# Optimization experiments

Hardware: AMD Instinct MI355X
Metric: run time of the kernel (lower is better)

Reference implementation:

```python
import jax, jax.numpy as jnp
import numpy as np

N = 4096
IN_F = 512
OUT_F = 1024
HEADS = 8
HEAD_F = OUT_F // HEADS  # 128
NEG_SLOPE = 0.2


def setup_inputs() -> dict:
    key = jax.random.key(0)
    ks = jax.random.split(key, 7)
    x = jax.random.normal(ks[0], (N, IN_F), dtype=jnp.float32)
    graph = jax.random.randint(ks[1], (N, N), 0, 2, dtype=jnp.int32)
    # xavier-normal-ish init scales
    W = jax.random.normal(ks[2], (HEADS, IN_F, HEAD_F), dtype=jnp.float32) * (2.0 / (IN_F + HEAD_F)) ** 0.5
    w_i = jax.random.normal(ks[3], (HEADS, HEAD_F, 1), dtype=jnp.float32) * (2.0 / (HEAD_F + 1)) ** 0.5
    w_j = jax.random.normal(ks[4], (HEADS, HEAD_F, 1), dtype=jnp.float32) * (2.0 / (HEAD_F + 1)) ** 0.5
    W_r = jax.random.normal(ks[5], (IN_F, HEAD_F * HEADS), dtype=jnp.float32) * (2.0 / (IN_F + HEAD_F * HEADS)) ** 0.5
    bias = jnp.zeros((OUT_F,), dtype=jnp.float32)
    return {"x": x, "graph": graph, "W": W, "w_i": w_i, "w_j": w_j, "W_r": W_r, "bias": bias}


def reference(x, graph, W, w_i, w_j, W_r, bias):
    # h: [H, N, F] = x @ W per head
    h = jnp.einsum('nm,hmf->hnf', x, W)
    coe_i = jnp.einsum('hnf,hfo->hno', h, w_i)              # [H, N, 1]
    coe_j = jnp.einsum('hnf,hfo->hno', h, w_j).transpose(0, 2, 1)  # [H, 1, N]
    coe = jax.nn.leaky_relu(coe_i + coe_j, negative_slope=NEG_SLOPE)  # [H, N, N]
    # adjacency mask: note the transpose as in the original (graph.t())
    mask = jnp.where(graph.T > 0, 0.0, -jnp.inf).astype(h.dtype)  # [N, N]
    att = jax.nn.softmax(coe + mask[None], axis=-1)          # [H, N, N]
    y = jnp.einsum('hnm,hmf->nhf', att, h)                   # [N, H, F]
    # mapped residual (in_features != head_features)
    y = y + (x @ W_r).reshape(-1, HEADS, HEAD_F)
    # concat heads
    y = y.reshape(-1, OUT_F)
    return y + bias
```

## Files before the change

### kernel.cpp

```cpp
#include <hip/hip_runtime.h>
#include <hip/hip_fp16.h>

typedef _Float16 f16;
typedef _Float16 f16x8 __attribute__((ext_vector_type(8)));
typedef _Float16 f16x2v __attribute__((ext_vector_type(2)));
typedef __fp16 h16x2 __attribute__((ext_vector_type(2)));
typedef float f32x4 __attribute__((ext_vector_type(4)));
typedef float f32x16 __attribute__((ext_vector_type(16)));

#define LOG2E 1.4426950408889634f
#define NSL 0.2f

__global__ __launch_bounds__(256) void k_a(const float* __restrict__ x,
                                           f16* __restrict__ xh2,
                                           const float* __restrict__ W,
                                           f16* __restrict__ Wht2,
                                           const float* __restrict__ Wr,
                                           f16* __restrict__ Wrt2,
                                           unsigned int* __restrict__ M2e) {
    __shared__ float tile[32][33];
    int bx = blockIdx.x;
    int tid = threadIdx.x;
    if (bx == 0 && tid < 8) M2e[tid] = 0x007FFFFFu;
    if (bx < 512) {
        int id = bx * 256 + tid;
        int row = id & 4095, kt = id >> 12;
        const float4* xs = (const float4*)(x + (size_t)row * 512 + kt * 16);
        float4 u0 = xs[0], u1 = xs[1], u2 = xs[2], u3 = xs[3];
        union { int4 a[2]; h16x2 p[8]; } px;
        px.p[0] = __builtin_amdgcn_cvt_pkrtz(u0.x, u0.y);
        px.p[1] = __builtin_amdgcn_cvt_pkrtz(u0.z, u0.w);
        px.p[2] = __builtin_amdgcn_cvt_pkrtz(u1.x, u1.y);
        px.p[3] = __builtin_amdgcn_cvt_pkrtz(u1.z, u1.w);
        px.p[4] = __builtin_amdgcn_cvt_pkrtz(u2.x, u2.y);
        px.p[5] = __builtin_amdgcn_cvt_pkrtz(u2.z, u2.w);
        px.p[6] = __builtin_amdgcn_cvt_pkrtz(u3.x, u3.y);
        px.p[7] = __builtin_amdgcn_cvt_pkrtz(u3.z, u3.w);
        int4* d = (int4*)(xh2 + ((size_t)kt * 4096 + row) * 16);
        d[0] = px.a[0]; d[1] = px.a[1];
    } else {
        const float* in; f16* out; int C, S, bxx, byy;
        if (bx < 1024) { int id = bx - 512;  in = W;  out = Wht2; C = 128;  S = 128;  bxx = id & 3;  byy = id >> 2; }
        else           { int id = bx - 1024; in = Wr; out = Wrt2; C = 1024; S = 1024; bxx = id & 31; byy = id >> 5; }
        int tx = tid & 31, ty = tid >> 5;
        int c0 = bxx * 32, r0 = byy * 32;
        for (int rr = ty; rr < 32; rr += 8)
            tile[rr][tx] = in[(r0 + rr) * C + c0 + tx];
        __syncthreads();
        for (int rr = ty; rr < 32; rr += 8) {
            int m = r0 + tx, f = c0 + rr;
            out[(size_t)((m >> 4) * S + f) * 16 + (m & 15)] = (f16)tile[tx][rr];
        }
    }
}

__global__ __launch_bounds__(256, 4) void k_b(const f16* __restrict__ xh2,
                                              const f16* __restrict__ Wht2,
                                              f16* __restrict__ hbT2,
                                              const float* __restrict__ wi,
                                              const float* __restrict__ wj,
                                              float* __restrict__ a2,
                                              float* __restrict__ b2,
                                              unsigned int* __restrict__ M2e,
                                              const int* __restrict__ graph,
                                              unsigned int* __restrict__ maskJ) {
    __shared__ float swi[128], swj[128];
    __shared__ float pwa[4][32], pwb[4][32];
    __shared__ unsigned long long bal[4][64];
    int bx = blockIdx.x;
    int tid = threadIdx.x;
    int w = tid >> 6, lane = tid & 63;

    if (bx >= 1024) {
        int gw = (bx - 1024) * 4 + w;
        int ti = gw & 63, tj = gw >> 6;
        int i0 = ti * 64, j0 = tj * 64;
        #pragma unroll 8
        for (int k = 0; k < 64; k++) {
            int g = graph[(j0 + k) * 4096 + i0 + lane];
            unsigned long long b = __ballot(g > 0);
            if (lane == 0) bal[w][k] = b;
        }
        __syncthreads();
        unsigned long long word = 0;
        #pragma unroll 8
        for (int k = 0; k < 64; k++) {
            word |= ((bal[w][k] >> lane) & 1ull) << k;
        }
        int jw = j0 >> 5;
        maskJ[(size_t)jw * 4096 + i0 + lane]       = (unsigned int)word;
        maskJ[(size_t)(jw + 1) * 4096 + i0 + lane] = (unsigned int)(word >> 32);
        return;
    }

    int h = bx & 7, jb = bx >> 3;
    int j0 = jb * 32;
    int ln = lane & 15, q = lane >> 4;
    if (tid < 128) { swi[tid] = wi[h * 128 + tid]; swj[tid] = wj[h * 128 + tid]; }
    __syncthreads();

    int ko = (q & 1) * 8;
    const f16* pa = Wht2 + ((size_t)(h * 512) * 8 + (size_t)(q >> 1) * 128 + w * 32 + ln) * 16 + ko;
    const f16* pb = xh2 + ((size_t)(q >> 1) * 4096 + j0 + ln) * 16 + ko;

    f32x4 acc00 = {}, acc01 = {}, acc10 = {}, acc11 = {};

    f16x8 ra0 = *(const f16x8*)(pa);
    f16x8 ra1 = *(const f16x8*)(pa + 256);
    f16x8 rb0 = *(const f16x8*)(pb);
    f16x8 rb1 = *(const f16x8*)(pb + 256);

    for (int kk = 0; kk < 8; kk++) {
        f16x8 sa0 = *(const f16x8*)(pa + 4096);
        f16x8 sa1 = *(const f16x8*)(pa + 4096 + 256);
        f16x8 sb0 = *(const f16x8*)(pb + 131072);
        f16x8 sb1 = *(const f16x8*)(pb + 131072 + 256);
        acc00 = __builtin_amdgcn_mfma_f32_16x16x32_f16(ra0, rb0, acc00, 0, 0, 0);
        acc01 = __builtin_amdgcn_mfma_f32_16x16x32_f16(ra0, rb1, acc01, 0, 0, 0);
        acc10 = __builtin_amdgcn_mfma_f32_16x16x32_f16(ra1, rb0, acc10, 0, 0, 0);
        acc11 = __builtin_amdgcn_mfma_f32_16x16x32_f16(ra1, rb1, acc11, 0, 0, 0);
        pa += 8192; pb += 262144;
        ra0 = *(const f16x8*)(pa);
        ra1 = *(const f16x8*)(pa + 256);
        rb0 = *(const f16x8*)(pb);
        rb1 = *(const f16x8*)(pb + 256);
        acc00 = __builtin_amdgcn_mfma_f32_16x16x32_f16(sa0, sb0, acc00, 0, 0, 0);
        acc01 = __builtin_amdgcn_mfma_f32_16x16x32_f16(sa0, sb1, acc01, 0, 0, 0);
        acc10 = __builtin_amdgcn_mfma_f32_16x16x32_f16(sa1, sb0, acc10, 0, 0, 0);
        acc11 = __builtin_amdgcn_mfma_f32_16x16x32_f16(sa1, sb1, acc11, 0, 0, 0);
    }

    size_t hb = (size_t)h * 524288 + (size_t)(j0 >> 4) * 2048;
    #pragma unroll
    for (int r = 0; r < 4; r++) {
        int f0 = w * 32 + q * 4 + r;
        hbT2[hb + f0 * 16 + ln]                 = (f16)acc00[r];
        hbT2[hb + 2048 + f0 * 16 + ln]          = (f16)acc01[r];
        hbT2[hb + (f0 + 16) * 16 + ln]          = (f16)acc10[r];
        hbT2[hb + 2048 + (f0 + 16) * 16 + ln]   = (f16)acc11[r];
    }

    float pa0 = 0.f, pb0 = 0.f, pa1 = 0.f, pb1 = 0.f;
    #pragma unroll
    for (int r = 0; r < 4; r++) {
        int f0 = w * 32 + q * 4 + r;
        float w0 = swi[f0], jv0 = swj[f0];
        float w1 = swi[f0 + 16], jv1 = swj[f0 + 16];
        pa0 += acc00[r] * w0 + acc10[r] * w1;
        pb0 += acc00[r] * jv0 + acc10[r] * jv1;
        pa1 += acc01[r] * w0 + acc11[r] * w1;
        pb1 += acc01[r] * jv0 + acc11[r] * jv1;
    }
    pa0 += __shfl_xor(pa0, 16); pa0 += __shfl_xor(pa0, 32);
    pb0 += __shfl_xor(pb0, 16); pb0 += __shfl_xor(pb0, 32);
    pa1 += __shfl_xor(pa1, 16); pa1 += __shfl_xor(pa1, 32);
    pb1 += __shfl_xor(pb1, 16); pb1 += __shfl_xor(pb1, 32);
    if (lane < 16) {
        pwa[w][ln] = pa0;      pwb[w][ln] = pb0;
        pwa[w][16 + ln] = pa1; pwb[w][16 + ln] = pb1;
    }
    __syncthreads();
    if (tid < 32) {
        int jj = tid;
        float pav = (pwa[0][jj] + pwa[1][jj]) + (pwa[2][jj] + pwa[3][jj]);
        float pbv = (pwb[0][jj] + pwb[1][jj]) + (pwb[2][jj] + pwb[3][jj]);
        a2[h * 4096 + j0 + jj] = pav * LOG2E;
        float bb = pbv * LOG2E;
        b2[h * 4096 + j0 + jj] = bb;
        float m = bb;
        m = fmaxf(m, __shfl_xor(m, 1, 32));
        m = fmaxf(m, __shfl_xor(m, 2, 32));
        m = fmaxf(m, __shfl_xor(m, 4, 32));
        m = fmaxf(m, __shfl_xor(m, 8, 32));
        m = fmaxf(m, __shfl_xor(m, 16, 32));
        if (jj == 0) {
            unsigned u = __float_as_uint(m);
            unsigned enc = (u & 0x80000000u) ? ~u : (u | 0x80000000u);
            atomicMax(&M2e[h], enc);
        }
    }
}

#define PGEN2(af, m8, qv, qw)                                                        \
    {                                                                                \
        union { int4 i4; unsigned u[4]; } uv, uw;                                    \
        uv.i4 = (qv); uw.i4 = (qw);                                                  \
        f16x2v dl = {(_Float16)0, (_Float16)0};                                      \
        _Pragma("unroll")                                                            \
        for (int p = 0; p < 4; p++) {                                                \
            union { unsigned u; f16x2v v; } b1, b2x, mm;                             \
            b1.u = uv.u[p]; b2x.u = uw.u[p];                                         \
            f16x2v pr1 = Ap1 * b1.v;                                                 \
            f16x2v pr2 = Ap2 * b2x.v;                                                \
            mm.v = __builtin_elementwise_max(pr1, pr2);                              \
            int mlo = -(int)(((m8) >> (2 * p)) & 1u);                                \
            int mhi = -(int)(((m8) >> (2 * p + 1)) & 1u);                            \
            unsigned comb = ((unsigned)mlo & 0xFFFFu) | ((unsigned)mhi & 0xFFFF0000u);\
            mm.u &= comb;                                                            \
            af.u[p] = mm.u;                                                          \
            dl += mm.v;                                                              \
        }                                                                            \
        dsum += (float)dl.x + (float)dl.y;                                           \
    }

#define PUTACC(dp, off, accv)                                                    \
    {                                                                            \
        union { f32x16 v; f32x4 q[4]; } t; t.v = (accv);                         \
        *(f32x4*)((dp) + (off))      = t.q[0];                                   \
        *(f32x4*)((dp) + (off) + 4)  = t.q[1];                                   \
        *(f32x4*)((dp) + (off) + 8)  = t.q[2];                                   \
        *(f32x4*)((dp) + (off) + 12) = t.q[3];                                   \
    }

#define ADDACC(dp, off, accv)                                                    \
    {                                                                            \
        union { f32x16 v; f32x4 q[4]; } t; t.v = (accv);                         \
        t.q[0] += *(const f32x4*)((dp) + (off));                                 \
        t.q[1] += *(const f32x4*)((dp) + (off) + 4);                             \
        t.q[2] += *(const f32x4*)((dp) + (off) + 8);                             \
        t.q[3] += *(const f32x4*)((dp) + (off) + 12);                            \
        (accv) = t.v;                                                            \
    }

__global__ __launch_bounds__(256, 4) void k_main(const f16* __restrict__ xh2,
                                                 const f16* __restrict__ hbT2,
                                                 const f16* __restrict__ Wrt2,
                                                 const unsigned int* __restrict__ maskJ,
                                                 const float* __restrict__ a2,
                                                 const float* __restrict__ b2,
                                                 const unsigned int* __restrict__ M2e,
                                                 const float* __restrict__ bias,
                                                 float* __restrict__ out) {
    __shared__ char smem[35328];
    __shared__ float dred[128];

    unsigned int* mlds = (unsigned int*)smem;
    unsigned int* bvlds = (unsigned int*)(smem + 16512);
    unsigned int* bwlds = (unsigned int*)(smem + 24704);

    int bx = blockIdx.x;
    int h = bx & 7, it = bx >> 3;
    int i0 = it * 32;
    int tid = threadIdx.x;
    int w = tid >> 6, lane = tid & 63;
    int l31 = lane & 31, half = lane >> 5;
    int i = i0 + l31;

    unsigned enc = M2e[h];
    unsigned um = (enc & 0x80000000u) ? (enc & 0x7FFFFFFFu) : ~enc;
    float M2 = __uint_as_float(um);

    {
        const float2* bsrc = (const float2*)(b2 + h * 4096);
        #pragma unroll
        for (int c = 0; c < 8; c++) {
            int p = tid + c * 256;
            float2 tb = bsrc[p];
            float t0 = tb.x - M2, t1 = tb.y - M2;
            union { h16x2 pp; unsigned ii; } k1, k2;
            k1.pp = __builtin_amdgcn_cvt_pkrtz(exp2f(t0), exp2f(t1));
            k2.pp = __builtin_amdgcn_cvt_pkrtz(exp2f(NSL * t0), exp2f(NSL * t1));
            bvlds[p] = k1.ii;
            bwlds[p] = k2.ii;
        }
        #pragma unroll
        for (int c = 0; c < 16; c++) {
            int e = tid + c * 256;
            int jw = e >> 5, ii = e & 31;
            mlds[ii * 129 + jw] = maskJ[(size_t)jw * 4096 + i0 + ii];
        }
    }

    float av = a2[h * 4096 + i];
    float uu = av + M2;
    float m2v = fmaxf(uu, NSL * uu);
    union { h16x2 pp; f16x2v v; } apk;
    apk.pp = __builtin_amdgcn_cvt_pkrtz(exp2f(uu - m2v), exp2f(NSL * uu - m2v));
    f16x2v Ap1 = {apk.v.x, apk.v.x};
    f16x2v Ap2 = {apk.v.y, apk.v.y};

    f32x16 acc0 = {}, acc1 = {}, acc2 = {}, acc3 = {};
    float dsum = 0.f;

    int J0 = w * 1024;
    const f16* bb = hbT2 + (size_t)h * 524288 + ((size_t)(J0 >> 4) * 128 + l31) * 16 + half * 8;
    const unsigned int* bpv = bvlds + (J0 >> 1) + half * 4;
    const unsigned int* bpw = bwlds + (J0 >> 1) + half * 4;
    const unsigned int* mrow = mlds + l31 * 129 + (J0 >> 5);

    int sh0 = half << 3;
    int sh1 = 16 + (half << 3);

    __syncthreads();

    f16x8 fa0 = *(const f16x8*)(bb);
    f16x8 fa1 = *(const f16x8*)(bb + 512);
    f16x8 fa2 = *(const f16x8*)(bb + 1024);
    f16x8 fa3 = *(const f16x8*)(bb + 1536);
    int4 qv0 = ((const int4*)(bpv))[0];
    int4 qw0 = ((const int4*)(bpw))[0];
    unsigned mwc = mrow[0];

    for (int tp = 0; tp < 32; tp++) {
        int t0 = tp * 2;
        const f16* s1 = bb + (size_t)(t0 + 1) * 2048;
        f16x8 fb0 = *(const f16x8*)(s1);
        f16x8 fb1 = *(const f16x8*)(s1 + 512);
        f16x8 fb2 = *(const f16x8*)(s1 + 1024);
        f16x8 fb3 = *(const f16x8*)(s1 + 1536);
        int4 qv1 = *(const int4*)(bpv + (t0 + 1) * 8);
        int4 qw1 = *(const int4*)(bpw + (t0 + 1) * 8);
        unsigned mwn = mrow[tp + 1];

        {
            union { f16x8 v; unsigned u[4]; } af;
            PGEN2(af, mwc >> sh0, qv0, qw0);
            acc0 = __builtin_amdgcn_mfma_f32_32x32x16_f16(af.v, fa0, acc0, 0, 0, 0);
            acc1 = __builtin_amdgcn_mfma_f32_32x32x16_f16(af.v, fa1, acc1, 0, 0, 0);
            acc2 = __builtin_amdgcn_mfma_f32_32x32x16_f16(af.v, fa2, acc2, 0, 0, 0);
            acc3 = __builtin_amdgcn_mfma_f32_32x32x16_f16(af.v, fa3, acc3, 0, 0, 0);
        }

        const f16* s2 = bb + (size_t)(t0 + 2) * 2048;
        fa0 = *(const f16x8*)(s2);
        fa1 = *(const f16x8*)(s2 + 512);
        fa2 = *(const f16x8*)(s2 + 1024);
        fa3 = *(const f16x8*)(s2 + 1536);
        qv0 = *(const int4*)(bpv + (t0 + 2) * 8);
        qw0 = *(const int4*)(bpw + (t0 + 2) * 8);

        {
            union { f16x8 v; unsigned u[4]; } af;
            PGEN2(af, mwc >> sh1, qv1, qw1);
            acc0 = __builtin_amdgcn_mfma_f32_32x32x16_f16(af.v, fb0, acc0, 0, 0, 0);
            acc1 = __builtin_amdgcn_mfma_f32_32x32x16_f16(af.v, fb1, acc1, 0, 0, 0);
            acc2 = __builtin_amdgcn_mfma_f32_32x32x16_f16(af.v, fb2, acc2, 0, 0, 0);
            acc3 = __builtin_amdgcn_mfma_f32_32x32x16_f16(af.v, fb3, acc3, 0, 0, 0);
        }
        mwc = mwn;
    }

    dsum += __shfl(dsum, lane ^ 32);
    if (lane < 32) dred[w * 32 + l31] = dsum;
    __syncthreads();
    {
        #pragma unroll
        for (int r = 0; r < 16; r++) {
            int row = (r & 3) + 8 * (r >> 2) + 4 * half;
            float s = dred[row] + dred[32 + row] + dred[64 + row] + dred[96 + row];
            float inv = 1.0f / s;
            acc0[r] *= inv; acc1[r] *= inv; acc2[r] *= inv; acc3[r] *= inv;
        }
    }

    {
        #pragma unroll
        for (int kt = 0; kt < 8; kt++) {
            int ktt = w * 8 + kt;
            f16x8 ax = *(const f16x8*)(xh2 + ((size_t)ktt * 4096 + i) * 16 + half * 8);
            const f16* wb = Wrt2 + ((size_t)ktt * 1024 + h * 128 + l31) * 16 + half * 8;
            acc0 = __builtin_amdgcn_mfma_f32_32x32x16_f16(ax, *(const f16x8*)(wb), acc0, 0, 0, 0);
            acc1 = __builtin_amdgcn_mfma_f32_32x32x16_f16(ax, *(const f16x8*)(wb + 512), acc1, 0, 0, 0);
            acc2 = __builtin_amdgcn_mfma_f32_32x32x16_f16(ax, *(const f16x8*)(wb + 1024), acc2, 0, 0, 0);
            acc3 = __builtin_amdgcn_mfma_f32_32x32x16_f16(ax, *(const f16x8*)(wb + 1536), acc3, 0, 0, 0);
        }
    }

    float* xredb = (float*)smem;
    __syncthreads();
    if (w >= 2) {
        float* dp = xredb + (w - 2) * 4352 + lane * 68;
        PUTACC(dp, 0, acc0); PUTACC(dp, 16, acc1); PUTACC(dp, 32, acc2); PUTACC(dp, 48, acc3);
    }
    __syncthreads();
    if (w < 2) {
        const float* dp = xredb + w * 4352 + lane * 68;
        ADDACC(dp, 0, acc0); ADDACC(dp, 16, acc1); ADDACC(dp, 32, acc2); ADDACC(dp, 48, acc3);
    }
    __syncthreads();
    if (w == 1) {
        float* dp = xredb + lane * 68;
        PUTACC(dp, 0, acc0); PUTACC(dp, 16, acc1); PUTACC(dp, 32, acc2); PUTACC(dp, 48, acc3);
    }
    __syncthreads();
    if (w == 0) {
        const float* dp = xredb + lane * 68;
        ADDACC(dp, 0, acc0); ADDACC(dp, 16, acc1); ADDACC(dp, 32, acc2); ADDACC(dp, 48, acc3);
        #pragma unroll
        for (int n = 0; n < 4; n++) {
            union { f32x16 v; f32x4 q[4]; } t;
            t.v = (n == 0) ? acc0 : (n == 1) ? acc1 : (n == 2) ? acc2 : acc3;
            int col = h * 128 + n * 32 + l31;
            float bv = bias[col];
            #pragma unroll
            for (int r = 0; r < 16; r++) {
                int row = i0 + (r & 3) + 8 * (r >> 2) + 4 * half;
                out[(size_t)row * 1024 + col] = t.v[r] + bv;
            }
        }
    }
}

extern "C" void kernel_launch(void* const* d_in, const int* in_sizes, int n_in,
                              void* d_out, int out_size, void* d_ws, size_t ws_size,
                              hipStream_t stream) {
    (void)in_sizes; (void)n_in; (void)out_size; (void)ws_size;
    const float* x     = (const float*)d_in[0];
    const int*   graph = (const int*)d_in[1];
    const float* W     = (const float*)d_in[2];
    const float* wi    = (const float*)d_in[3];
    const float* wj    = (const float*)d_in[4];
    const float* Wr    = (const float*)d_in[5];
    const float* bias  = (const float*)d_in[6];
    float* out = (float*)d_out;

    char* ws = (char*)d_ws;
    unsigned int* maskJ = (unsigned int*)ws;
    f16* hbT2  = (f16*)(ws + (2u << 20));
    f16* Wht2  = (f16*)(ws + (10u << 20));
    f16* Wrt2  = (f16*)(ws + (11u << 20));
    f16* xh2   = (f16*)(ws + (12u << 20));
    float* a2    = (float*)(ws + (16u << 20));
    float* b2    = a2 + 8 * 4096;
    unsigned int* M2e = (unsigned int*)(b2 + 8 * 4096);

    hipLaunchKernelGGL(k_a, dim3(1536), dim3(256), 0, stream, x, xh2, W, Wht2, Wr, Wrt2, M2e);
    hipLaunchKernelGGL(k_b, dim3(2048), dim3(256), 0, stream, xh2, Wht2, hbT2,
                       wi, wj, a2, b2, M2e, graph, maskJ);
    hipLaunchKernelGGL(k_main, dim3(1024), dim3(256), 0, stream, xh2, hbT2, Wrt2, maskJ,
                       a2, b2, M2e, bias, out);
}
```

Baseline: 222.6 us.

## Process 64 query rows per block to reuse loaded h tiles twice

Each k_main block now handles 64 rows instead of 32, with two sets of MFMA accumulators (low and high halves) sharing the same B fragments of hbT2 and the same exp tables held in LDS. This halves the global traffic for the value matrix and the per-block exp-table setup, and halves the grid to 512 blocks. In exchange, register pressure doubles, which forces launch bounds down to 2 blocks per SM. LDS use also grows, and with fewer blocks on a 256-CU part occupancy and load balance may suffer.

```diff
diff --git a/kernel.cpp b/kernel.cpp
--- a/kernel.cpp
+++ b/kernel.cpp
@@ -181,7 +181,7 @@
     }
 }
 
-#define PGEN2(af, m8, qv, qw)                                                        \
+#define PGEN2(af, m8, qv, qw, A1, A2, DS)                                            \
     {                                                                                \
         union { int4 i4; unsigned u[4]; } uv, uw;                                    \
         uv.i4 = (qv); uw.i4 = (qw);                                                  \
@@ -190,8 +190,8 @@
         for (int p = 0; p < 4; p++) {                                                \
             union { unsigned u; f16x2v v; } b1, b2x, mm;                             \
             b1.u = uv.u[p]; b2x.u = uw.u[p];                                         \
-            f16x2v pr1 = Ap1 * b1.v;                                                 \
-            f16x2v pr2 = Ap2 * b2x.v;                                                \
+            f16x2v pr1 = (A1) * b1.v;                                                \
+            f16x2v pr2 = (A2) * b2x.v;                                               \
             mm.v = __builtin_elementwise_max(pr1, pr2);                              \
             int mlo = -(int)(((m8) >> (2 * p)) & 1u);                                \
             int mhi = -(int)(((m8) >> (2 * p + 1)) & 1u);                            \
@@ -200,7 +200,7 @@
             af.u[p] = mm.u;                                                          \
             dl += mm.v;                                                              \
         }                                                                            \
-        dsum += (float)dl.x + (float)dl.y;                                           \
+        DS += (float)dl.x + (float)dl.y;                                             \
     }
 
 #define PUTACC(dp, off, accv)                                                    \
@@ -222,7 +222,7 @@
         (accv) = t.v;                                                            \
     }
 
-__global__ __launch_bounds__(256, 4) void k_main(const f16* __restrict__ xh2,
+__global__ __launch_bounds__(256, 2) void k_main(const f16* __restrict__ xh2,
                                                  const f16* __restrict__ hbT2,
                                                  const f16* __restrict__ Wrt2,
                                                  const unsigned int* __restrict__ maskJ,
@@ -231,16 +231,16 @@
                                                  const unsigned int* __restrict__ M2e,
                                                  const float* __restrict__ bias,
                                                  float* __restrict__ out) {
-    __shared__ char smem[35328];
-    __shared__ float dred[128];
+    __shared__ char smem[49664];
+    __shared__ float dred[256];
 
     unsigned int* mlds = (unsigned int*)smem;
-    unsigned int* bvlds = (unsigned int*)(smem + 16512);
-    unsigned int* bwlds = (unsigned int*)(smem + 24704);
+    unsigned int* bvlds = (unsigned int*)(smem + 33024);
+    unsigned int* bwlds = (unsigned int*)(smem + 41216);
 
     int bx = blockIdx.x;
     int h = bx & 7, it = bx >> 3;
-    int i0 = it * 32;
+    int i0 = it * 64;
     int tid = threadIdx.x;
     int w = tid >> 6, lane = tid & 63;
     int l31 = lane & 31, half = lane >> 5;
@@ -264,29 +264,36 @@
             bwlds[p] = k2.ii;
         }
         #pragma unroll
-        for (int c = 0; c < 16; c++) {
+        for (int c = 0; c < 32; c++) {
             int e = tid + c * 256;
-            int jw = e >> 5, ii = e & 31;
+            int jw = e >> 6, ii = e & 63;
             mlds[ii * 129 + jw] = maskJ[(size_t)jw * 4096 + i0 + ii];
         }
     }
 
-    float av = a2[h * 4096 + i];
-    float uu = av + M2;
-    float m2v = fmaxf(uu, NSL * uu);
-    union { h16x2 pp; f16x2v v; } apk;
-    apk.pp = __builtin_amdgcn_cvt_pkrtz(exp2f(uu - m2v), exp2f(NSL * uu - m2v));
-    f16x2v Ap1 = {apk.v.x, apk.v.x};
-    f16x2v Ap2 = {apk.v.y, apk.v.y};
-
-    f32x16 acc0 = {}, acc1 = {}, acc2 = {}, acc3 = {};
-    float dsum = 0.f;
+    float avL = a2[h * 4096 + i];
+    float avH = a2[h * 4096 + i + 32];
+    float uuL = avL + M2, uuH = avH + M2;
+    float mvL = fmaxf(uuL, NSL * uuL);
+    float mvH = fmaxf(uuH, NSL * uuH);
+    union { h16x2 pp; f16x2v v; } apL, apH;
+    apL.pp = __builtin_amdgcn_cvt_pkrtz(exp2f(uuL - mvL), exp2f(NSL * uuL - mvL));
+    apH.pp = __builtin_amdgcn_cvt_pkrtz(exp2f(uuH - mvH), exp2f(NSL * uuH - mvH));
+    f16x2v ApL1 = {apL.v.x, apL.v.x};
+    f16x2v ApL2 = {apL.v.y, apL.v.y};
+    f16x2v ApH1 = {apH.v.x, apH.v.x};
+    f16x2v ApH2 = {apH.v.y, apH.v.y};
+
+    f32x16 accL0 = {}, accL1 = {}, accL2 = {}, accL3 = {};
+    f32x16 accH0 = {}, accH1 = {}, accH2 = {}, accH3 = {};
+    float dsumL = 0.f, dsumH = 0.f;
 
     int J0 = w * 1024;
     const f16* bb = hbT2 + (size_t)h * 524288 + ((size_t)(J0 >> 4) * 128 + l31) * 16 + half * 8;
     const unsigned int* bpv = bvlds + (J0 >> 1) + half * 4;
     const unsigned int* bpw = bwlds + (J0 >> 1) + half * 4;
-    const unsigned int* mrow = mlds + l31 * 129 + (J0 >> 5);
+    const unsigned int* mrowL = mlds + l31 * 129 + (J0 >> 5);
+    const unsigned int* mrowH = mlds + (l31 + 32) * 129 + (J0 >> 5);
 
     int sh0 = half << 3;
     int sh1 = 16 + (half << 3);
@@ -299,7 +306,8 @@
     f16x8 fa3 = *(const f16x8*)(bb + 1536);
     int4 qv0 = ((const int4*)(bpv))[0];
     int4 qw0 = ((const int4*)(bpw))[0];
-    unsigned mwc = mrow[0];
+    unsigned mwcL = mrowL[0];
+    unsigned mwcH = mrowH[0];
 
     for (int tp = 0; tp < 32; tp++) {
         int t0 = tp * 2;
@@ -310,15 +318,24 @@
         f16x8 fb3 = *(const f16x8*)(s1 + 1536);
         int4 qv1 = *(const int4*)(bpv + (t0 + 1) * 8);
         int4 qw1 = *(const int4*)(bpw + (t0 + 1) * 8);
-        unsigned mwn = mrow[tp + 1];
+        unsigned mwnL = mrowL[tp + 1];
+        unsigned mwnH = mrowH[tp + 1];
 
         {
             union { f16x8 v; unsigned u[4]; } af;
-            PGEN2(af, mwc >> sh0, qv0, qw0);
-            acc0 = __builtin_amdgcn_mfma_f32_32x32x16_f16(af.v, fa0, acc0, 0, 0, 0);
-            acc1 = __builtin_amdgcn_mfma_f32_32x32x16_f16(af.v, fa1, acc1, 0, 0, 0);
-            acc2 = __builtin_amdgcn_mfma_f32_32x32x16_f16(af.v, fa2, acc2, 0, 0, 0);
-            acc3 = __builtin_amdgcn_mfma_f32_32x32x16_f16(af.v, fa3, acc3, 0, 0, 0);
+            PGEN2(af, mwcL >> sh0, qv0, qw0, ApL1, ApL2, dsumL);
+            accL0 = __builtin_amdgcn_mfma_f32_32x32x16_f16(af.v, fa0, accL0, 0, 0, 0);
+            accL1 = __builtin_amdgcn_mfma_f32_32x32x16_f16(af.v, fa1, accL1, 0, 0, 0);
+            accL2 = __builtin_amdgcn_mfma_f32_32x32x16_f16(af.v, fa2, accL2, 0, 0, 0);
+            accL3 = __builtin_amdgcn_mfma_f32_32x32x16_f16(af.v, fa3, accL3, 0, 0, 0);
+        }
+        {
+            union { f16x8 v; unsigned u[4]; } af;
+            PGEN2(af, mwcH >> sh0, qv0, qw0, ApH1, ApH2, dsumH);
+            accH0 = __builtin_amdgcn_mfma_f32_32x32x16_f16(af.v, fa0, accH0, 0, 0, 0);
+            accH1 = __builtin_amdgcn_mfma_f32_32x32x16_f16(af.v, fa1, accH1, 0, 0, 0);
+            accH2 = __builtin_amdgcn_mfma_f32_32x32x16_f16(af.v, fa2, accH2, 0, 0, 0);
+            accH3 = __builtin_amdgcn_mfma_f32_32x32x16_f16(af.v, fa3, accH3, 0, 0, 0);
         }
 
         const f16* s2 = bb + (size_t)(t0 + 2) * 2048;
@@ -331,25 +348,41 @@
 
         {
             union { f16x8 v; unsigned u[4]; } af;
-            PGEN2(af, mwc >> sh1, qv1, qw1);
-            acc0 = __builtin_amdgcn_mfma_f32_32x32x16_f16(af.v, fb0, acc0, 0, 0, 0);
-            acc1 = __builtin_amdgcn_mfma_f32_32x32x16_f16(af.v, fb1, acc1, 0, 0, 0);
-            acc2 = __builtin_amdgcn_mfma_f32_32x32x16_f16(af.v, fb2, acc2, 0, 0, 0);
-            acc3 = __builtin_amdgcn_mfma_f32_32x32x16_f16(af.v, fb3, acc3, 0, 0, 0);
-        }
-        mwc = mwn;
-    }
-
-    dsum += __shfl(dsum, lane ^ 32);
-    if (lane < 32) dred[w * 32 + l31] = dsum;
+            PGEN2(af, mwcL >> sh1, qv1, qw1, ApL1, ApL2, dsumL);
+            accL0 = __builtin_amdgcn_mfma_f32_32x32x16_f16(af.v, fb0, accL0, 0, 0, 0);
+            accL1 = __builtin_amdgcn_mfma_f32_32x32x16_f16(af.v, fb1, accL1, 0, 0, 0);
+            accL2 = __builtin_amdgcn_mfma_f32_32x32x16_f16(af.v, fb2, accL2, 0, 0, 0);
+            accL3 = __builtin_amdgcn_mfma_f32_32x32x16_f16(af.v, fb3, accL3, 0, 0, 0);
+        }
+        {
+            union { f16x8 v; unsigned u[4]; } af;
+            PGEN2(af, mwcH >> sh1, qv1, qw1, ApH1, ApH2, dsumH);
+            accH0 = __builtin_amdgcn_mfma_f32_32x32x16_f16(af.v, fb0, accH0, 0, 0, 0);
+            accH1 = __builtin_amdgcn_mfma_f32_32x32x16_f16(af.v, fb1, accH1, 0, 0, 0);
+            accH2 = __builtin_amdgcn_mfma_f32_32x32x16_f16(af.v, fb2, accH2, 0, 0, 0);
+            accH3 = __builtin_amdgcn_mfma_f32_32x32x16_f16(af.v, fb3, accH3, 0, 0, 0);
+        }
+        mwcL = mwnL;
+        mwcH = mwnH;
+    }
+
+    dsumL += __shfl(dsumL, lane ^ 32);
+    dsumH += __shfl(dsumH, lane ^ 32);
+    if (lane < 32) {
+        dred[w * 64 + l31] = dsumL;
+        dred[w * 64 + 32 + l31] = dsumH;
+    }
     __syncthreads();
     {
         #pragma unroll
         for (int r = 0; r < 16; r++) {
             int row = (r & 3) + 8 * (r >> 2) + 4 * half;
-            float s = dred[row] + dred[32 + row] + dred[64 + row] + dred[96 + row];
-            float inv = 1.0f / s;
-            acc0[r] *= inv; acc1[r] *= inv; acc2[r] *= inv; acc3[r] *= inv;
+            float sL = dred[row] + dred[64 + row] + dred[128 + row] + dred[192 + row];
+            float sH = dred[32 + row] + dred[96 + row] + dred[160 + row] + dred[224 + row];
+            float invL = 1.0f / sL;
+            float invH = 1.0f / sH;
+            accL0[r] *= invL; accL1[r] *= invL; accL2[r] *= invL; accL3[r] *= invL;
+            accH0[r] *= invH; accH1[r] *= invH; accH2[r] *= invH; accH3[r] *= invH;
         }
     }
 
@@ -357,44 +390,87 @@
         #pragma unroll
         for (int kt = 0; kt < 8; kt++) {
             int ktt = w * 8 + kt;
-            f16x8 ax = *(const f16x8*)(xh2 + ((size_t)ktt * 4096 + i) * 16 + half * 8);
+            f16x8 axL = *(const f16x8*)(xh2 + ((size_t)ktt * 4096 + i) * 16 + half * 8);
+            f16x8 axH = *(const f16x8*)(xh2 + ((size_t)ktt * 4096 + i + 32) * 16 + half * 8);
             const f16* wb = Wrt2 + ((size_t)ktt * 1024 + h * 128 + l31) * 16 + half * 8;
-            acc0 = __builtin_amdgcn_mfma_f32_32x32x16_f16(ax, *(const f16x8*)(wb), acc0, 0, 0, 0);
-            acc1 = __builtin_amdgcn_mfma_f32_32x32x16_f16(ax, *(const f16x8*)(wb + 512), acc1, 0, 0, 0);
-            acc2 = __builtin_amdgcn_mfma_f32_32x32x16_f16(ax, *(const f16x8*)(wb + 1024), acc2, 0, 0, 0);
-            acc3 = __builtin_amdgcn_mfma_f32_32x32x16_f16(ax, *(const f16x8*)(wb + 1536), acc3, 0, 0, 0);
+            f16x8 wb0 = *(const f16x8*)(wb);
+            f16x8 wb1 = *(const f16x8*)(wb + 512);
+            f16x8 wb2 = *(const f16x8*)(wb + 1024);
+            f16x8 wb3 = *(const f16x8*)(wb + 1536);
+            accL0 = __builtin_amdgcn_mfma_f32_32x32x16_f16(axL, wb0, accL0, 0, 0, 0);
+            accL1 = __builtin_amdgcn_mfma_f32_32x32x16_f16(axL, wb1, accL1, 0, 0, 0);
+            accL2 = __builtin_amdgcn_mfma_f32_32x32x16_f16(axL, wb2, accL2, 0, 0, 0);
+            accL3 = __builtin_amdgcn_mfma_f32_32x32x16_f16(axL, wb3, accL3, 0, 0, 0);
+            accH0 = __builtin_amdgcn_mfma_f32_32x32x16_f16(axH, wb0, accH0, 0, 0, 0);
+            accH1 = __builtin_amdgcn_mfma_f32_32x32x16_f16(axH, wb1, accH1, 0, 0, 0);
+            accH2 = __builtin_amdgcn_mfma_f32_32x32x16_f16(axH, wb2, accH2, 0, 0, 0);
+            accH3 = __builtin_amdgcn_mfma_f32_32x32x16_f16(axH, wb3, accH3, 0, 0, 0);
         }
     }
 
     float* xredb = (float*)smem;
+
     __syncthreads();
     if (w >= 2) {
         float* dp = xredb + (w - 2) * 4352 + lane * 68;
-        PUTACC(dp, 0, acc0); PUTACC(dp, 16, acc1); PUTACC(dp, 32, acc2); PUTACC(dp, 48, acc3);
+        PUTACC(dp, 0, accL0); PUTACC(dp, 16, accL1); PUTACC(dp, 32, accL2); PUTACC(dp, 48, accL3);
     }
     __syncthreads();
     if (w < 2) {
         const float* dp = xredb + w * 4352 + lane * 68;
-        ADDACC(dp, 0, acc0); ADDACC(dp, 16, acc1); ADDACC(dp, 32, acc2); ADDACC(dp, 48, acc3);
+        ADDACC(dp, 0, accL0); ADDACC(dp, 16, accL1); ADDACC(dp, 32, accL2); ADDACC(dp, 48, accL3);
     }
     __syncthreads();
     if (w == 1) {
         float* dp = xredb + lane * 68;
-        PUTACC(dp, 0, acc0); PUTACC(dp, 16, acc1); PUTACC(dp, 32, acc2); PUTACC(dp, 48, acc3);
+        PUTACC(dp, 0, accL0); PUTACC(dp, 16, accL1); PUTACC(dp, 32, accL2); PUTACC(dp, 48, accL3);
     }
     __syncthreads();
     if (w == 0) {
         const float* dp = xredb + lane * 68;
-        ADDACC(dp, 0, acc0); ADDACC(dp, 16, acc1); ADDACC(dp, 32, acc2); ADDACC(dp, 48, acc3);
+        ADDACC(dp, 0, accL0); ADDACC(dp, 16, accL1); ADDACC(dp, 32, accL2); ADDACC(dp, 48, accL3);
         #pragma unroll
         for (int n = 0; n < 4; n++) {
             union { f32x16 v; f32x4 q[4]; } t;
-            t.v = (n == 0) ? acc0 : (n == 1) ? acc1 : (n == 2) ? acc2 : acc3;
+            t.v = (n == 0) ? accL0 : (n == 1) ? accL1 : (n == 2) ? accL2 : accL3;
             int col = h * 128 + n * 32 + l31;
             float bv = bias[col];
             #pragma unroll
             for (int r = 0; r < 16; r++) {
                 int row = i0 + (r & 3) + 8 * (r >> 2) + 4 * half;
+                out[(size_t)row * 1024 + col] = t.v[r] + bv;
+            }
+        }
+    }
+
+    __syncthreads();
+    if (w >= 2) {
+        float* dp = xredb + (w - 2) * 4352 + lane * 68;
+        PUTACC(dp, 0, accH0); PUTACC(dp, 16, accH1); PUTACC(dp, 32, accH2); PUTACC(dp, 48, accH3);
+    }
+    __syncthreads();
+    if (w < 2) {
+        const float* dp = xredb + w * 4352 + lane * 68;
+        ADDACC(dp, 0, accH0); ADDACC(dp, 16, accH1); ADDACC(dp, 32, accH2); ADDACC(dp, 48, accH3);
+    }
+    __syncthreads();
+    if (w == 1) {
+        float* dp = xredb + lane * 68;
+        PUTACC(dp, 0, accH0); PUTACC(dp, 16, accH1); PUTACC(dp, 32, accH2); PUTACC(dp, 48, accH3);
+    }
+    __syncthreads();
+    if (w == 0) {
+        const float* dp = xredb + lane * 68;
+        ADDACC(dp, 0, accH0); ADDACC(dp, 16, accH1); ADDACC(dp, 32, accH2); ADDACC(dp, 48, accH3);
+        #pragma unroll
+        for (int n = 0; n < 4; n++) {
+            union { f32x16 v; f32x4 q[4]; } t;
+            t.v = (n == 0) ? accH0 : (n == 1) ? accH1 : (n == 2) ? accH2 : accH3;
+            int col = h * 128 + n * 32 + l31;
+            float bv = bias[col];
+            #pragma unroll
+            for (int r = 0; r < 16; r++) {
+                int row = i0 + 32 + (r & 3) + 8 * (r >> 2) + 4 * half;
                 out[(size_t)row * 1024 + col] = t.v[r] + bv;
             }
         }
@@ -427,6 +503,6 @@
     hipLaunchKernelGGL(k_a, dim3(1536), dim3(256), 0, stream, x, xh2, W, Wht2, Wr, Wrt2, M2e);
     hipLaunchKernelGGL(k_b, dim3(2048), dim3(256), 0, stream, xh2, Wht2, hbT2,
                        wi, wj, a2, b2, M2e, graph, maskJ);
-    hipLaunchKernelGGL(k_main, dim3(1024), dim3(256), 0, stream, xh2, hbT2, Wrt2, maskJ,
+    hipLaunchKernelGGL(k_main, dim3(512), dim3(256), 0, stream, xh2, hbT2, Wrt2, maskJ,
                        a2, b2, M2e, bias, out);
 }
```

Result: faster. 210.7 us (-5.4%).

## Restructure attention kernel to share probability tiles via LDS across 8 waves

Applied to the files above, without the earlier changes.

The main attention kernel now uses 512-thread blocks covering 64 rows. Each wave generates a slice of the masked softmax probabilities into double-buffered LDS, and all waves then run MFMAs on a 32-row by 32-feature output tile. The old per-wave split over the key dimension is gone, and with it the cross-wave accumulator reduction through LDS. The mask-packing path in k_b now does a per-thread strided gather instead of a ballot-and-transpose, with more blocks launched. This trades fewer redundant probability computations and smaller reductions for a barrier on every chunk and more LDS traffic.

```diff
diff --git a/kernel.cpp b/kernel.cpp
--- a/kernel.cpp
+++ b/kernel.cpp
@@ -66,30 +66,21 @@
                                               unsigned int* __restrict__ maskJ) {
     __shared__ float swi[128], swj[128];
     __shared__ float pwa[4][32], pwb[4][32];
-    __shared__ unsigned long long bal[4][64];
     int bx = blockIdx.x;
     int tid = threadIdx.x;
     int w = tid >> 6, lane = tid & 63;
 
     if (bx >= 1024) {
-        int gw = (bx - 1024) * 4 + w;
-        int ti = gw & 63, tj = gw >> 6;
-        int i0 = ti * 64, j0 = tj * 64;
-        #pragma unroll 8
-        for (int k = 0; k < 64; k++) {
-            int g = graph[(j0 + k) * 4096 + i0 + lane];
-            unsigned long long b = __ballot(g > 0);
-            if (lane == 0) bal[w][k] = b;
-        }
-        __syncthreads();
-        unsigned long long word = 0;
-        #pragma unroll 8
-        for (int k = 0; k < 64; k++) {
-            word |= ((bal[w][k] >> lane) & 1ull) << k;
-        }
-        int jw = j0 >> 5;
-        maskJ[(size_t)jw * 4096 + i0 + lane]       = (unsigned int)word;
-        maskJ[(size_t)(jw + 1) * 4096 + i0 + lane] = (unsigned int)(word >> 32);
+        int e = (bx - 1024) * 256 + tid;
+        int jw = e >> 12, ii = e & 4095;
+        const int* gp = graph + (size_t)(jw << 5) * 4096 + ii;
+        int gv[32];
+        #pragma unroll
+        for (int k = 0; k < 32; k++) gv[k] = gp[(size_t)k * 4096];
+        unsigned word = 0;
+        #pragma unroll
+        for (int k = 0; k < 32; k++) word |= (gv[k] > 0) ? (1u << k) : 0u;
+        maskJ[e] = word;
         return;
     }
 
@@ -181,7 +172,7 @@
     }
 }
 
-#define PGEN2(af, m8, qv, qw)                                                        \
+#define PGEN2(af, m8, qv, qw, A1, A2, DS)                                            \
     {                                                                                \
         union { int4 i4; unsigned u[4]; } uv, uw;                                    \
         uv.i4 = (qv); uw.i4 = (qw);                                                  \
@@ -190,8 +181,8 @@
         for (int p = 0; p < 4; p++) {                                                \
             union { unsigned u; f16x2v v; } b1, b2x, mm;                             \
             b1.u = uv.u[p]; b2x.u = uw.u[p];                                         \
-            f16x2v pr1 = Ap1 * b1.v;                                                 \
-            f16x2v pr2 = Ap2 * b2x.v;                                                \
+            f16x2v pr1 = (A1) * b1.v;                                                \
+            f16x2v pr2 = (A2) * b2x.v;                                               \
             mm.v = __builtin_elementwise_max(pr1, pr2);                              \
             int mlo = -(int)(((m8) >> (2 * p)) & 1u);                                \
             int mhi = -(int)(((m8) >> (2 * p + 1)) & 1u);                            \
@@ -200,29 +191,10 @@
             af.u[p] = mm.u;                                                          \
             dl += mm.v;                                                              \
         }                                                                            \
-        dsum += (float)dl.x + (float)dl.y;                                           \
-    }
-
-#define PUTACC(dp, off, accv)                                                    \
-    {                                                                            \
-        union { f32x16 v; f32x4 q[4]; } t; t.v = (accv);                         \
-        *(f32x4*)((dp) + (off))      = t.q[0];                                   \
-        *(f32x4*)((dp) + (off) + 4)  = t.q[1];                                   \
-        *(f32x4*)((dp) + (off) + 8)  = t.q[2];                                   \
-        *(f32x4*)((dp) + (off) + 12) = t.q[3];                                   \
-    }
-
-#define ADDACC(dp, off, accv)                                                    \
-    {                                                                            \
-        union { f32x16 v; f32x4 q[4]; } t; t.v = (accv);                         \
-        t.q[0] += *(const f32x4*)((dp) + (off));                                 \
-        t.q[1] += *(const f32x4*)((dp) + (off) + 4);                             \
-        t.q[2] += *(const f32x4*)((dp) + (off) + 8);                             \
-        t.q[3] += *(const f32x4*)((dp) + (off) + 12);                            \
-        (accv) = t.v;                                                            \
-    }
-
-__global__ __launch_bounds__(256, 4) void k_main(const f16* __restrict__ xh2,
+        DS += (float)dl.x + (float)dl.y;                                             \
+    }
+
+__global__ __launch_bounds__(512, 4) void k_main(const f16* __restrict__ xh2,
                                                  const f16* __restrict__ hbT2,
                                                  const f16* __restrict__ Wrt2,
                                                  const unsigned int* __restrict__ maskJ,
@@ -232,19 +204,25 @@
                                                  const float* __restrict__ bias,
                                                  float* __restrict__ out) {
     __shared__ char smem[35328];
-    __shared__ float dred[128];
-
-    unsigned int* mlds = (unsigned int*)smem;
-    unsigned int* bvlds = (unsigned int*)(smem + 16512);
-    unsigned int* bwlds = (unsigned int*)(smem + 24704);
+    char* pb0 = smem;
+    char* pb1 = smem + 8192;
+    unsigned int* bvlds = (unsigned int*)(smem + 16384);
+    unsigned int* bwlds = (unsigned int*)(smem + 24576);
+    float* dred = (float*)(smem + 32768);
+    float* rsum = (float*)(smem + 34816);
 
     int bx = blockIdx.x;
     int h = bx & 7, it = bx >> 3;
-    int i0 = it * 32;
+    int i0 = it * 64;
     int tid = threadIdx.x;
     int w = tid >> 6, lane = tid & 63;
     int l31 = lane & 31, half = lane >> 5;
-    int i = i0 + l31;
+
+    int prow = tid & 63;
+    int poct = w;
+    int mshift = (poct & 3) * 8;
+    int fs = (w & 3) * 32;
+    int rh = (w >> 2) * 32;
 
     unsigned enc = M2e[h];
     unsigned um = (enc & 0x80000000u) ? (enc & 0x7FFFFFFFu) : ~enc;
@@ -253,8 +231,8 @@
     {
         const float2* bsrc = (const float2*)(b2 + h * 4096);
         #pragma unroll
-        for (int c = 0; c < 8; c++) {
-            int p = tid + c * 256;
+        for (int c = 0; c < 4; c++) {
+            int p = tid + c * 512;
             float2 tb = bsrc[p];
             float t0 = tb.x - M2, t1 = tb.y - M2;
             union { h16x2 pp; unsigned ii; } k1, k2;
@@ -263,142 +241,121 @@
             bvlds[p] = k1.ii;
             bwlds[p] = k2.ii;
         }
-        #pragma unroll
-        for (int c = 0; c < 16; c++) {
-            int e = tid + c * 256;
-            int jw = e >> 5, ii = e & 31;
-            mlds[ii * 129 + jw] = maskJ[(size_t)jw * 4096 + i0 + ii];
-        }
-    }
-
-    float av = a2[h * 4096 + i];
+    }
+
+    float av = a2[h * 4096 + i0 + prow];
     float uu = av + M2;
     float m2v = fmaxf(uu, NSL * uu);
     union { h16x2 pp; f16x2v v; } apk;
     apk.pp = __builtin_amdgcn_cvt_pkrtz(exp2f(uu - m2v), exp2f(NSL * uu - m2v));
     f16x2v Ap1 = {apk.v.x, apk.v.x};
     f16x2v Ap2 = {apk.v.y, apk.v.y};
-
-    f32x16 acc0 = {}, acc1 = {}, acc2 = {}, acc3 = {};
     float dsum = 0.f;
 
-    int J0 = w * 1024;
-    const f16* bb = hbT2 + (size_t)h * 524288 + ((size_t)(J0 >> 4) * 128 + l31) * 16 + half * 8;
-    const unsigned int* bpv = bvlds + (J0 >> 1) + half * 4;
-    const unsigned int* bpw = bwlds + (J0 >> 1) + half * 4;
-    const unsigned int* mrow = mlds + l31 * 129 + (J0 >> 5);
-
-    int sh0 = half << 3;
-    int sh1 = 16 + (half << 3);
-
-    __syncthreads();
-
-    f16x8 fa0 = *(const f16x8*)(bb);
-    f16x8 fa1 = *(const f16x8*)(bb + 512);
-    f16x8 fa2 = *(const f16x8*)(bb + 1024);
-    f16x8 fa3 = *(const f16x8*)(bb + 1536);
-    int4 qv0 = ((const int4*)(bpv))[0];
-    int4 qw0 = ((const int4*)(bpw))[0];
-    unsigned mwc = mrow[0];
-
-    for (int tp = 0; tp < 32; tp++) {
-        int t0 = tp * 2;
-        const f16* s1 = bb + (size_t)(t0 + 1) * 2048;
-        f16x8 fb0 = *(const f16x8*)(s1);
-        f16x8 fb1 = *(const f16x8*)(s1 + 512);
-        f16x8 fb2 = *(const f16x8*)(s1 + 1024);
-        f16x8 fb3 = *(const f16x8*)(s1 + 1536);
-        int4 qv1 = *(const int4*)(bpv + (t0 + 1) * 8);
-        int4 qw1 = *(const int4*)(bpw + (t0 + 1) * 8);
-        unsigned mwn = mrow[tp + 1];
-
-        {
-            union { f16x8 v; unsigned u[4]; } af;
-            PGEN2(af, mwc >> sh0, qv0, qw0);
-            acc0 = __builtin_amdgcn_mfma_f32_32x32x16_f16(af.v, fa0, acc0, 0, 0, 0);
-            acc1 = __builtin_amdgcn_mfma_f32_32x32x16_f16(af.v, fa1, acc1, 0, 0, 0);
-            acc2 = __builtin_amdgcn_mfma_f32_32x32x16_f16(af.v, fa2, acc2, 0, 0, 0);
-            acc3 = __builtin_amdgcn_mfma_f32_32x32x16_f16(af.v, fa3, acc3, 0, 0, 0);
-        }
-
-        const f16* s2 = bb + (size_t)(t0 + 2) * 2048;
-        fa0 = *(const f16x8*)(s2);
-        fa1 = *(const f16x8*)(s2 + 512);
-        fa2 = *(const f16x8*)(s2 + 1024);
-        fa3 = *(const f16x8*)(s2 + 1536);
-        qv0 = *(const int4*)(bpv + (t0 + 2) * 8);
-        qw0 = *(const int4*)(bpw + (t0 + 2) * 8);
-
-        {
-            union { f16x8 v; unsigned u[4]; } af;
-            PGEN2(af, mwc >> sh1, qv1, qw1);
-            acc0 = __builtin_amdgcn_mfma_f32_32x32x16_f16(af.v, fb0, acc0, 0, 0, 0);
-            acc1 = __builtin_amdgcn_mfma_f32_32x32x16_f16(af.v, fb1, acc1, 0, 0, 0);
-            acc2 = __builtin_amdgcn_mfma_f32_32x32x16_f16(af.v, fb2, acc2, 0, 0, 0);
-            acc3 = __builtin_amdgcn_mfma_f32_32x32x16_f16(af.v, fb3, acc3, 0, 0, 0);
-        }
-        mwc = mwn;
-    }
-
-    dsum += __shfl(dsum, lane ^ 32);
-    if (lane < 32) dred[w * 32 + l31] = dsum;
+    f32x16 acc = {};
+
+    int wroff = poct * 1024 + prow * 16;
+    const f16* bb = hbT2 + (size_t)h * 524288 + (size_t)(fs + l31) * 16 + half * 8;
+    const unsigned int* mpp = maskJ + (size_t)(poct >> 2) * 4096 + i0 + prow;
+
+    __syncthreads();
+
+#define PFB(C, B0, B1, B2, B3)                                           \
+    B0 = *(const f16x8*)(bb + (size_t)((C) * 4 + 0) * 2048);             \
+    B1 = *(const f16x8*)(bb + (size_t)((C) * 4 + 1) * 2048);             \
+    B2 = *(const f16x8*)(bb + (size_t)((C) * 4 + 2) * 2048);             \
+    B3 = *(const f16x8*)(bb + (size_t)((C) * 4 + 3) * 2048);
+
+#define PGC(C, PB, MW)                                                   \
+    {                                                                    \
+        int4 qv = *(const int4*)(bvlds + (C) * 32 + poct * 4);           \
+        int4 qw = *(const int4*)(bwlds + (C) * 32 + poct * 4);           \
+        union { f16x8 v; unsigned u[4]; int4 i4; } af;                   \
+        unsigned m8v = (MW) >> mshift;                                   \
+        PGEN2(af, m8v, qv, qw, Ap1, Ap2, dsum);                          \
+        *(int4*)((PB) + wroff) = af.i4;                                  \
+    }
+
+#define MMC(PB, B0, B1, B2, B3)                                          \
+    {                                                                    \
+        const f16* pr = (const f16*)(PB) + (size_t)(rh + l31) * 8;       \
+        f16x8 a0 = *(const f16x8*)(pr + (0 + half) * 512);               \
+        f16x8 a1 = *(const f16x8*)(pr + (2 + half) * 512);               \
+        f16x8 a2f = *(const f16x8*)(pr + (4 + half) * 512);              \
+        f16x8 a3 = *(const f16x8*)(pr + (6 + half) * 512);               \
+        __builtin_amdgcn_s_setprio(1);                                   \
+        acc = __builtin_amdgcn_mfma_f32_32x32x16_f16(a0, B0, acc, 0, 0, 0); \
+        acc = __builtin_amdgcn_mfma_f32_32x32x16_f16(a1, B1, acc, 0, 0, 0); \
+        acc = __builtin_amdgcn_mfma_f32_32x32x16_f16(a2f, B2, acc, 0, 0, 0);\
+        acc = __builtin_amdgcn_mfma_f32_32x32x16_f16(a3, B3, acc, 0, 0, 0); \
+        __builtin_amdgcn_s_setprio(0);                                   \
+    }
+
+    f16x8 bA0, bA1, bA2, bA3, bB0, bB1, bB2, bB3;
+    PFB(0, bA0, bA1, bA2, bA3)
+    PFB(1, bB0, bB1, bB2, bB3)
+    unsigned mwE = mpp[0];
+    unsigned mwO = mpp[8192];
+    PGC(0, pb0, mwE)
+    mwE = mpp[2 * 8192];
+    __syncthreads();
+
+    #pragma unroll 1
+    for (int c = 0; c < 62; c += 2) {
+        PGC(c + 1, pb1, mwO)
+        mwO = mpp[(size_t)(c + 3) * 8192];
+        MMC(pb0, bA0, bA1, bA2, bA3)
+        PFB(c + 2, bA0, bA1, bA2, bA3)
+        __syncthreads();
+        PGC(c + 2, pb0, mwE)
+        mwE = mpp[(size_t)(c + 4) * 8192];
+        MMC(pb1, bB0, bB1, bB2, bB3)
+        PFB(c + 3, bB0, bB1, bB2, bB3)
+        __syncthreads();
+    }
+    PGC(63, pb1, mwO)
+    MMC(pb0, bA0, bA1, bA2, bA3)
+    __syncthreads();
+    MMC(pb1, bB0, bB1, bB2, bB3)
+
+    dred[poct * 64 + prow] = dsum;
+    __syncthreads();
+    if (tid < 64) {
+        float s = 0.f;
+        #pragma unroll
+        for (int o = 0; o < 8; o++) s += dred[o * 64 + tid];
+        rsum[tid] = 1.0f / s;
+    }
     __syncthreads();
     {
         #pragma unroll
         for (int r = 0; r < 16; r++) {
-            int row = (r & 3) + 8 * (r >> 2) + 4 * half;
-            float s = dred[row] + dred[32 + row] + dred[64 + row] + dred[96 + row];
-            float inv = 1.0f / s;
-            acc0[r] *= inv; acc1[r] *= inv; acc2[r] *= inv; acc3[r] *= inv;
+            int rowl = (r & 3) + 8 * (r >> 2) + 4 * half + rh;
+            acc[r] *= rsum[rowl];
         }
     }
 
     {
-        #pragma unroll
-        for (int kt = 0; kt < 8; kt++) {
-            int ktt = w * 8 + kt;
-            f16x8 ax = *(const f16x8*)(xh2 + ((size_t)ktt * 4096 + i) * 16 + half * 8);
-            const f16* wb = Wrt2 + ((size_t)ktt * 1024 + h * 128 + l31) * 16 + half * 8;
-            acc0 = __builtin_amdgcn_mfma_f32_32x32x16_f16(ax, *(const f16x8*)(wb), acc0, 0, 0, 0);
-            acc1 = __builtin_amdgcn_mfma_f32_32x32x16_f16(ax, *(const f16x8*)(wb + 512), acc1, 0, 0, 0);
-            acc2 = __builtin_amdgcn_mfma_f32_32x32x16_f16(ax, *(const f16x8*)(wb + 1024), acc2, 0, 0, 0);
-            acc3 = __builtin_amdgcn_mfma_f32_32x32x16_f16(ax, *(const f16x8*)(wb + 1536), acc3, 0, 0, 0);
-        }
-    }
-
-    float* xredb = (float*)smem;
-    __syncthreads();
-    if (w >= 2) {
-        float* dp = xredb + (w - 2) * 4352 + lane * 68;
-        PUTACC(dp, 0, acc0); PUTACC(dp, 16, acc1); PUTACC(dp, 32, acc2); PUTACC(dp, 48, acc3);
-    }
-    __syncthreads();
-    if (w < 2) {
-        const float* dp = xredb + w * 4352 + lane * 68;
-        ADDACC(dp, 0, acc0); ADDACC(dp, 16, acc1); ADDACC(dp, 32, acc2); ADDACC(dp, 48, acc3);
-    }
-    __syncthreads();
-    if (w == 1) {
-        float* dp = xredb + lane * 68;
-        PUTACC(dp, 0, acc0); PUTACC(dp, 16, acc1); PUTACC(dp, 32, acc2); PUTACC(dp, 48, acc3);
-    }
-    __syncthreads();
-    if (w == 0) {
-        const float* dp = xredb + lane * 68;
-        ADDACC(dp, 0, acc0); ADDACC(dp, 16, acc1); ADDACC(dp, 32, acc2); ADDACC(dp, 48, acc3);
-        #pragma unroll
-        for (int n = 0; n < 4; n++) {
-            union { f32x16 v; f32x4 q[4]; } t;
-            t.v = (n == 0) ? acc0 : (n == 1) ? acc1 : (n == 2) ? acc2 : acc3;
-            int col = h * 128 + n * 32 + l31;
-            float bv = bias[col];
-            #pragma unroll
-            for (int r = 0; r < 16; r++) {
-                int row = i0 + (r & 3) + 8 * (r >> 2) + 4 * half;
-                out[(size_t)row * 1024 + col] = t.v[r] + bv;
-            }
-        }
-    }
+        #pragma unroll 4
+        for (int kt = 0; kt < 32; kt++) {
+            f16x8 ax = *(const f16x8*)(xh2 + ((size_t)kt * 4096 + i0 + rh + l31) * 16 + half * 8);
+            f16x8 wb = *(const f16x8*)(Wrt2 + ((size_t)kt * 1024 + h * 128 + fs + l31) * 16 + half * 8);
+            acc = __builtin_amdgcn_mfma_f32_32x32x16_f16(ax, wb, acc, 0, 0, 0);
+        }
+    }
+
+    {
+        int col = h * 128 + fs + l31;
+        float bv = bias[col];
+        #pragma unroll
+        for (int r = 0; r < 16; r++) {
+            int row = i0 + rh + (r & 3) + 8 * (r >> 2) + 4 * half;
+            out[(size_t)row * 1024 + col] = acc[r] + bv;
+        }
+    }
+#undef PFB
+#undef PGC
+#undef MMC
 }
 
 extern "C" void kernel_launch(void* const* d_in, const int* in_sizes, int n_in,
@@ -425,8 +382,8 @@
     unsigned int* M2e = (unsigned int*)(b2 + 8 * 4096);
 
     hipLaunchKernelGGL(k_a, dim3(1536), dim3(256), 0, stream, x, xh2, W, Wht2, Wr, Wrt2, M2e);
-    hipLaunchKernelGGL(k_b, dim3(2048), dim3(256), 0, stream, xh2, Wht2, hbT2,
+    hipLaunchKernelGGL(k_b, dim3(3072), dim3(256), 0, stream, xh2, Wht2, hbT2,
                        wi, wj, a2, b2, M2e, graph, maskJ);
-    hipLaunchKernelGGL(k_main, dim3(1024), dim3(256), 0, stream, xh2, hbT2, Wrt2, maskJ,
+    hipLaunchKernelGGL(k_main, dim3(512), dim3(512), 0, stream, xh2, hbT2, Wrt2, maskJ,
                        a2, b2, M2e, bias, out);
 }
```

Result: faster. 193.7 us (-13.0%).
